# Kernel optimization log

Measured on AMD Instinct MI355X. Metric: run time of the kernel, lower is better.

The kernel has to match this reference:

```python
import jax, jax.numpy as jnp
import numpy as np

NUM_HEADS = 16
LN_EPS = 1e-5


def _layer_norm(x, w, b, eps=LN_EPS):
    m = jnp.mean(x, axis=-1, keepdims=True)
    v = jnp.var(x, axis=-1, keepdims=True)
    return (x - m) / jnp.sqrt(v + eps) * w + b


def setup_inputs() -> dict:
    key = jax.random.key(0)
    L, D, DFF, B, S = 16, 1024, 4096, 4, 1024
    ks = jax.random.split(key, 6)
    w_scale = 0.02
    return {
        "x": jax.random.normal(ks[0], (B, S, D), jnp.float32),
        "qkv_w": jax.random.normal(ks[1], (L, 3 * D, D), jnp.float32) * w_scale,
        "qkv_b": jnp.zeros((L, 3 * D), jnp.float32),
        "out_w": jax.random.normal(ks[2], (L, D, D), jnp.float32) * w_scale,
        "out_b": jnp.zeros((L, D), jnp.float32),
        "w1": jax.random.normal(ks[3], (L, DFF, D), jnp.float32) * w_scale,
        "b1": jnp.zeros((L, DFF), jnp.float32),
        "w2": jax.random.normal(ks[4], (L, D, DFF), jnp.float32) * w_scale,
        "b2": jnp.zeros((L, D), jnp.float32),
        "ln1_w": jnp.ones((L, D), jnp.float32),
        "ln1_b": jnp.zeros((L, D), jnp.float32),
        "ln2_w": jnp.ones((L, D), jnp.float32),
        "ln2_b": jnp.zeros((L, D), jnp.float32),
    }


def reference(x, qkv_w, qkv_b, out_w, out_b, w1, b1, w2, b2, ln1_w, ln1_b, ln2_w, ln2_b):
    # T2STransformer.process_prompt: stack of T2SBlocks with causal attention.
    B, S, D = x.shape
    H = NUM_HEADS
    dh = D // H
    # causal additive bias [1,1,S,S]; True on/below diagonal -> attend
    causal = jnp.tril(jnp.ones((S, S), bool))
    bias = jnp.where(causal, 0.0, -jnp.inf).astype(x.dtype)[None, None]
    scale = 1.0 / np.sqrt(dh)

    def step(h, p):
        (qw, qb, ow, ob, mw1, mb1, mw2, mb2, l1w, l1b, l2w, l2b) = p
        qkv = h @ qw.T + qb                      # [B,S,3D]
        q, k, v = jnp.split(qkv, 3, axis=-1)
        q = q.reshape(B, S, H, dh).transpose(0, 2, 1, 3)  # [B,H,S,dh]
        k = k.reshape(B, S, H, dh).transpose(0, 2, 1, 3)
        v = v.reshape(B, S, H, dh).transpose(0, 2, 1, 3)
        scores = jnp.einsum("bhqd,bhkd->bhqk", q, k) * scale + bias
        attn = jax.nn.softmax(scores, axis=-1)
        ctx = jnp.einsum("bhqk,bhkd->bhqd", attn, v)
        ctx = ctx.transpose(0, 2, 1, 3).reshape(B, S, D)
        h = h + (ctx @ ow.T + ob)
        h = _layer_norm(h, l1w, l1b)
        mlp = jax.nn.relu(h @ mw1.T + mb1) @ mw2.T + mb2
        h = _layer_norm(h + mlp, l2w, l2b)
        return h, None

    params = (qkv_w, qkv_b, out_w, out_b, w1, b1, w2, b2, ln1_w, ln1_b, ln2_w, ln2_b)
    out, _ = jax.lax.scan(step, x, params)
    return out
```

## Files before the change

kernel.cpp:

```cpp
#include <hip/hip_runtime.h>
#include <hip/hip_bf16.h>

typedef float f32x4 __attribute__((ext_vector_type(4)));
typedef __bf16 bf16x8 __attribute__((ext_vector_type(8)));
typedef unsigned short ushort_t;

__device__ __forceinline__ unsigned short f2bf(float f) {
    unsigned int u = __builtin_bit_cast(unsigned int, f);
    u += 0x7fffu + ((u >> 16) & 1u);
    return (unsigned short)(u >> 16);
}

#define GCAST(p) ((const __attribute__((address_space(1))) void*)(p))
#define LCAST(p) ((__attribute__((address_space(3))) void*)(p))

__device__ __forceinline__ bf16x8 ldsw(const unsigned short* T, int row, int bcol) {
    return *reinterpret_cast<const bf16x8*>(
        reinterpret_cast<const char*>(T) + row * 128 + (bcol ^ ((row & 7) << 4)));
}

__device__ __forceinline__ int xcd_swizzle(int bid, int nwg) {
    int cpx = nwg >> 3;
    return (bid & 7) * cpx + (bid >> 3);
}

__global__ __launch_bounds__(256) void convert_weights_kernel(
    const float* __restrict__ qw, const float* __restrict__ ow,
    const float* __restrict__ w1, const float* __restrict__ w2,
    unsigned short* __restrict__ dst)
{
    int i = blockIdx.x * 256 + threadIdx.x;
    const float* src; int off;
    if (i < 786432)       { src = qw; off = i; }
    else if (i < 1048576) { src = ow; off = i - 786432; }
    else if (i < 2097152) { src = w1; off = i - 1048576; }
    else                  { src = w2; off = i - 2097152; }
    float4 v = ((const float4*)src)[off];
    ushort4 u;
    u.x = f2bf(v.x); u.y = f2bf(v.y); u.z = f2bf(v.z); u.w = f2bf(v.w);
    ((ushort4*)dst)[i] = u;
}

__global__ __launch_bounds__(256) void gemm_kernel(
    const unsigned short* __restrict__ A, const unsigned short* __restrict__ W,
    const float* __restrict__ bias, void* __restrict__ Cout,
    int N, int K, int relu, int out_bf16)
{
    __shared__ alignas(16) unsigned short As[128][64];
    __shared__ alignas(16) unsigned short Bs[128][64];

    const int tid  = threadIdx.x;
    const int nwg  = gridDim.x * gridDim.y;
    const int swz  = xcd_swizzle(blockIdx.y * gridDim.x + blockIdx.x, nwg);
    const int bn   = swz % gridDim.x, bm = swz / gridDim.x;
    const int wave = tid >> 6, lane = tid & 63;
    const int wm   = (wave >> 1) * 64, wn = (wave & 1) * 64;
    const int l15  = lane & 15, quad = lane >> 4;
    const int srow = lane >> 3;
    const int scol = (lane & 7) * 8;

    f32x4 acc[4][4];
#pragma unroll
    for (int i = 0; i < 4; i++)
#pragma unroll
        for (int j = 0; j < 4; j++) acc[i][j] = f32x4{0.f, 0.f, 0.f, 0.f};

    const unsigned short* Abase = A + (size_t)(bm * 128) * K;
    const unsigned short* Wbase = W + (size_t)(bn * 128) * K;

    for (int k0 = 0; k0 < K; k0 += 64) {
        __syncthreads();
#pragma unroll
        for (int i = 0; i < 4; i++) {
            int r0 = (i * 4 + wave) * 8;
            __builtin_amdgcn_global_load_lds(
                GCAST(&Abase[(size_t)(r0 + srow) * K + k0 + scol]),
                LCAST(&As[r0][0]), 16, 0, 0);
            __builtin_amdgcn_global_load_lds(
                GCAST(&Wbase[(size_t)(r0 + srow) * K + k0 + scol]),
                LCAST(&Bs[r0][0]), 16, 0, 0);
        }
        __syncthreads();

#pragma unroll
        for (int ks = 0; ks < 2; ks++) {
            bf16x8 a[4], b[4];
#pragma unroll
            for (int mt = 0; mt < 4; mt++)
                a[mt] = *reinterpret_cast<const bf16x8*>(&As[wm + mt * 16 + l15][ks * 32 + quad * 8]);
#pragma unroll
            for (int nt = 0; nt < 4; nt++)
                b[nt] = *reinterpret_cast<const bf16x8*>(&Bs[wn + nt * 16 + l15][ks * 32 + quad * 8]);
#pragma unroll
            for (int mt = 0; mt < 4; mt++)
#pragma unroll
                for (int nt = 0; nt < 4; nt++)
                    acc[mt][nt] = __builtin_amdgcn_mfma_f32_16x16x32_bf16(
                        a[mt], b[nt], acc[mt][nt], 0, 0, 0);
        }
    }

    float* Cf = (float*)Cout;
    unsigned short* Cb = (unsigned short*)Cout;
#pragma unroll
    for (int nt = 0; nt < 4; nt++) {
        int gn = bn * 128 + wn + nt * 16 + l15;
        float bv = bias[gn];
#pragma unroll
        for (int mt = 0; mt < 4; mt++) {
            int gm0 = bm * 128 + wm + mt * 16 + quad * 4;
#pragma unroll
            for (int r = 0; r < 4; r++) {
                float v = acc[mt][nt][r] + bv;
                if (relu) v = fmaxf(v, 0.f);
                if (out_bf16) Cb[(size_t)(gm0 + r) * N + gn] = f2bf(v);
                else          Cf[(size_t)(gm0 + r) * N + gn] = v;
            }
        }
    }
}

__global__ __launch_bounds__(256) void gemm_splitk_kernel(
    const unsigned short* __restrict__ A, const unsigned short* __restrict__ W,
    const float* __restrict__ bias, float* __restrict__ C0, float* __restrict__ C1,
    int N, int K)
{
    __shared__ alignas(16) unsigned short As[128][64];
    __shared__ alignas(16) unsigned short Bs[128][64];

    const int tid  = threadIdx.x;
    const int nwg  = gridDim.x * gridDim.y;
    const int swz  = xcd_swizzle(blockIdx.y * gridDim.x + blockIdx.x, nwg);
    const int bn   = swz % gridDim.x, bm = swz / gridDim.x;
    const int kz   = blockIdx.z;
    const int kbeg = kz * (K >> 1);
    const int kend = kbeg + (K >> 1);
    const int wave = tid >> 6, lane = tid & 63;
    const int wm   = (wave >> 1) * 64, wn = (wave & 1) * 64;
    const int l15  = lane & 15, quad = lane >> 4;
    const int srow = lane >> 3;
    const int scol = (lane & 7) * 8;

    f32x4 acc[4][4];
#pragma unroll
    for (int i = 0; i < 4; i++)
#pragma unroll
        for (int j = 0; j < 4; j++) acc[i][j] = f32x4{0.f, 0.f, 0.f, 0.f};

    const unsigned short* Abase = A + (size_t)(bm * 128) * K;
    const unsigned short* Wbase = W + (size_t)(bn * 128) * K;

    for (int k0 = kbeg; k0 < kend; k0 += 64) {
        __syncthreads();
#pragma unroll
        for (int i = 0; i < 4; i++) {
            int r0 = (i * 4 + wave) * 8;
            __builtin_amdgcn_global_load_lds(
                GCAST(&Abase[(size_t)(r0 + srow) * K + k0 + scol]),
                LCAST(&As[r0][0]), 16, 0, 0);
            __builtin_amdgcn_global_load_lds(
                GCAST(&Wbase[(size_t)(r0 + srow) * K + k0 + scol]),
                LCAST(&Bs[r0][0]), 16, 0, 0);
        }
        __syncthreads();

#pragma unroll
        for (int ks = 0; ks < 2; ks++) {
            bf16x8 a[4], b[4];
#pragma unroll
            for (int mt = 0; mt < 4; mt++)
                a[mt] = *reinterpret_cast<const bf16x8*>(&As[wm + mt * 16 + l15][ks * 32 + quad * 8]);
#pragma unroll
            for (int nt = 0; nt < 4; nt++)
                b[nt] = *reinterpret_cast<const bf16x8*>(&Bs[wn + nt * 16 + l15][ks * 32 + quad * 8]);
#pragma unroll
            for (int mt = 0; mt < 4; mt++)
#pragma unroll
                for (int nt = 0; nt < 4; nt++)
                    acc[mt][nt] = __builtin_amdgcn_mfma_f32_16x16x32_bf16(
                        a[mt], b[nt], acc[mt][nt], 0, 0, 0);
        }
    }

    float* Cf = kz ? C1 : C0;
#pragma unroll
    for (int nt = 0; nt < 4; nt++) {
        int gn = bn * 128 + wn + nt * 16 + l15;
        float bv = kz ? 0.f : bias[gn];
#pragma unroll
        for (int mt = 0; mt < 4; mt++) {
            int gm0 = bm * 128 + wm + mt * 16 + quad * 4;
#pragma unroll
            for (int r = 0; r < 4; r++)
                Cf[(size_t)(gm0 + r) * N + gn] = acc[mt][nt][r] + bv;
        }
    }
}

__global__ __launch_bounds__(256) void attn_kernel(
    const unsigned short* __restrict__ qkv, unsigned short* __restrict__ ctx)
{
    const int qt = blockIdx.x;
    const int bh = blockIdx.y;
    const int b  = bh >> 4, h = bh & 15;
    const int tid = threadIdx.x, wave = tid >> 6, lane = tid & 63;
    const int l15 = lane & 15, quad = lane >> 4;
    const int srow = lane >> 3;
    const int scolz = ((lane & 7) ^ srow) * 8;
    const float scale = 0.125f;

    __shared__ alignas(16) unsigned short Qs[64][64];
    __shared__ alignas(16) unsigned short Ks[64][64];
    __shared__ alignas(16) unsigned short Vt[64][64];
    __shared__ alignas(16) unsigned short Ps[64][64];

    const unsigned short* qbase = qkv + (size_t)(b * 1024 + qt * 64) * 3072 + h * 64;
#pragma unroll
    for (int i = 0; i < 2; i++) {
        int r0 = (i * 4 + wave) * 8;
        __builtin_amdgcn_global_load_lds(
            GCAST(&qbase[(size_t)(r0 + srow) * 3072 + scolz]),
            LCAST(&Qs[r0][0]), 16, 0, 0);
    }

    f32x4 O[4];
#pragma unroll
    for (int dt = 0; dt < 4; dt++) O[dt] = f32x4{0.f, 0.f, 0.f, 0.f};
    float m_run[4], l_run[4];
#pragma unroll
    for (int r = 0; r < 4; r++) { m_run[r] = -__builtin_inff(); l_run[r] = 0.f; }

    const int q_row_base = qt * 64 + wave * 16;

    for (int j = 0; j <= qt; j++) {
        __syncthreads();
        const unsigned short* kbase = qkv + (size_t)(b * 1024 + j * 64) * 3072 + 1024 + h * 64;
        const unsigned short* vbase = qkv + (size_t)(b * 1024 + j * 64) * 3072 + 2048 + h * 64;
#pragma unroll
        for (int i = 0; i < 2; i++) {
            int r0 = (i * 4 + wave) * 8;
            __builtin_amdgcn_global_load_lds(
                GCAST(&kbase[(size_t)(r0 + srow) * 3072 + scolz]),
                LCAST(&Ks[r0][0]), 16, 0, 0);
        }
#pragma unroll
        for (int i = 0; i < 4; i++) {
            int idx = tid + i * 256;
            int k = idx >> 4, c4 = (idx & 15) * 4;
            ushort4 vv = *(const ushort4*)&vbase[(size_t)k * 3072 + c4];
            char* vt = (char*)Vt;
            int klo = (k & 7) * 2;
            int kch = (k >> 3) << 4;
            const unsigned short* vp = (const unsigned short*)&vv;
#pragma unroll
            for (int j2 = 0; j2 < 4; j2++) {
                int d = c4 + j2;
                *(unsigned short*)(vt + d * 128 + ((kch ^ ((d & 7) << 4)) | klo)) = vp[j2];
            }
        }
        __syncthreads();

        f32x4 Sc[4];
#pragma unroll
        for (int nt = 0; nt < 4; nt++) Sc[nt] = f32x4{0.f, 0.f, 0.f, 0.f};
        __builtin_amdgcn_s_setprio(1);
#pragma unroll
        for (int ks = 0; ks < 2; ks++) {
            bf16x8 aq = ldsw(&Qs[0][0], wave * 16 + l15, ks * 64 + quad * 16);
#pragma unroll
            for (int nt = 0; nt < 4; nt++) {
                bf16x8 bk = ldsw(&Ks[0][0], nt * 16 + l15, ks * 64 + quad * 16);
                Sc[nt] = __builtin_amdgcn_mfma_f32_16x16x32_bf16(aq, bk, Sc[nt], 0, 0, 0);
            }
        }
        __builtin_amdgcn_s_setprio(0);

#pragma unroll
        for (int nt = 0; nt < 4; nt++)
#pragma unroll
            for (int r = 0; r < 4; r++) Sc[nt][r] *= scale;

        if (j == qt) {
#pragma unroll
            for (int r = 0; r < 4; r++) {
                int qg = q_row_base + quad * 4 + r;
#pragma unroll
                for (int nt = 0; nt < 4; nt++) {
                    int kg = j * 64 + nt * 16 + l15;
                    if (kg > qg) Sc[nt][r] = -__builtin_inff();
                }
            }
        }

        float alpha[4];
#pragma unroll
        for (int r = 0; r < 4; r++) {
            float mx = -__builtin_inff();
#pragma unroll
            for (int nt = 0; nt < 4; nt++) mx = fmaxf(mx, Sc[nt][r]);
#pragma unroll
            for (int off = 1; off < 16; off <<= 1) mx = fmaxf(mx, __shfl_xor(mx, off));
            float mnew = fmaxf(m_run[r], mx);
            alpha[r] = __expf(m_run[r] - mnew);
            m_run[r] = mnew;
        }

#pragma unroll
        for (int r = 0; r < 4; r++) {
            float sum = 0.f;
#pragma unroll
            for (int nt = 0; nt < 4; nt++) {
                float p = __expf(Sc[nt][r] - m_run[r]);
                Sc[nt][r] = p;
                sum += p;
            }
#pragma unroll
            for (int off = 1; off < 16; off <<= 1) sum += __shfl_xor(sum, off);
            l_run[r] = l_run[r] * alpha[r] + sum;
        }

#pragma unroll
        for (int dt = 0; dt < 4; dt++)
#pragma unroll
            for (int r = 0; r < 4; r++) O[dt][r] *= alpha[r];

        {
            char* ps = (char*)Ps;
#pragma unroll
            for (int nt = 0; nt < 4; nt++)
#pragma unroll
                for (int r = 0; r < 4; r++) {
                    int row = wave * 16 + quad * 4 + r;
                    int col = nt * 16 + l15;
                    *(unsigned short*)(ps + row * 128 + ((col * 2) ^ ((row & 7) << 4)))
                        = f2bf(Sc[nt][r]);
                }
        }

        __builtin_amdgcn_s_setprio(1);
#pragma unroll
        for (int ks = 0; ks < 2; ks++) {
            bf16x8 ap = ldsw(&Ps[0][0], wave * 16 + l15, ks * 64 + quad * 16);
#pragma unroll
            for (int dt = 0; dt < 4; dt++) {
                bf16x8 bv = ldsw(&Vt[0][0], dt * 16 + l15, ks * 64 + quad * 16);
                O[dt] = __builtin_amdgcn_mfma_f32_16x16x32_bf16(ap, bv, O[dt], 0, 0, 0);
            }
        }
        __builtin_amdgcn_s_setprio(0);
    }

    unsigned short* obase = ctx + (size_t)(b * 1024 + qt * 64 + wave * 16) * 1024 + h * 64;
#pragma unroll
    for (int r = 0; r < 4; r++) {
        float inv = 1.f / l_run[r];
#pragma unroll
        for (int dt = 0; dt < 4; dt++)
            obase[(size_t)(quad * 4 + r) * 1024 + dt * 16 + l15] = f2bf(O[dt][r] * inv);
    }
}

__global__ __launch_bounds__(256) void ln_residual_kernel(
    float* __restrict__ h, unsigned short* __restrict__ hb,
    const float* __restrict__ r, const float* __restrict__ r2,
    const float* __restrict__ w, const float* __restrict__ b)
{
    const int row = blockIdx.x;
    const int tid = threadIdx.x;
    const int lane = tid & 63, wave = tid >> 6;

    float4 hv = *(float4*)&h[(size_t)row * 1024 + tid * 4];
    float4 rv = *(const float4*)&r[(size_t)row * 1024 + tid * 4];
    float4 r2v = *(const float4*)&r2[(size_t)row * 1024 + tid * 4];
    float x0 = hv.x + rv.x + r2v.x, x1 = hv.y + rv.y + r2v.y;
    float x2 = hv.z + rv.z + r2v.z, x3 = hv.w + rv.w + r2v.w;

    float s  = x0 + x1 + x2 + x3;
    float s2 = x0 * x0 + x1 * x1 + x2 * x2 + x3 * x3;
#pragma unroll
    for (int off = 32; off >= 1; off >>= 1) {
        s  += __shfl_xor(s, off);
        s2 += __shfl_xor(s2, off);
    }
    __shared__ float ls[4], ls2[4];
    if (lane == 0) { ls[wave] = s; ls2[wave] = s2; }
    __syncthreads();
    s  = ls[0] + ls[1] + ls[2] + ls[3];
    s2 = ls2[0] + ls2[1] + ls2[2] + ls2[3];

    const float inv_n = 1.f / 1024.f;
    float mean = s * inv_n;
    float var  = s2 * inv_n - mean * mean;
    float rstd = rsqrtf(var + 1e-5f);

    float4 wv = *(const float4*)&w[tid * 4];
    float4 bv = *(const float4*)&b[tid * 4];
    float4 out;
    out.x = (x0 - mean) * rstd * wv.x + bv.x;
    out.y = (x1 - mean) * rstd * wv.y + bv.y;
    out.z = (x2 - mean) * rstd * wv.z + bv.z;
    out.w = (x3 - mean) * rstd * wv.w + bv.w;
    *(float4*)&h[(size_t)row * 1024 + tid * 4] = out;
    ushort4 ub;
    ub.x = f2bf(out.x); ub.y = f2bf(out.y); ub.z = f2bf(out.z); ub.w = f2bf(out.w);
    *(ushort4*)&hb[(size_t)row * 1024 + tid * 4] = ub;
}

__global__ __launch_bounds__(256) void copy_convert_kernel(
    const float* __restrict__ in, float* __restrict__ h, unsigned short* __restrict__ hb)
{
    int i = blockIdx.x * 256 + threadIdx.x;
    float4 v = ((const float4*)in)[i];
    ((float4*)h)[i] = v;
    ushort4 u;
    u.x = f2bf(v.x); u.y = f2bf(v.y); u.z = f2bf(v.z); u.w = f2bf(v.w);
    ((ushort4*)hb)[i] = u;
}

extern "C" void kernel_launch(void* const* d_in, const int* in_sizes, int n_in,
                              void* d_out, int out_size, void* d_ws, size_t ws_size,
                              hipStream_t stream)
{
    const float* x     = (const float*)d_in[0];
    const float* qkv_w = (const float*)d_in[1];
    const float* qkv_b = (const float*)d_in[2];
    const float* out_w = (const float*)d_in[3];
    const float* out_b = (const float*)d_in[4];
    const float* w1    = (const float*)d_in[5];
    const float* b1    = (const float*)d_in[6];
    const float* w2    = (const float*)d_in[7];
    const float* b2    = (const float*)d_in[8];
    const float* ln1w  = (const float*)d_in[9];
    const float* ln1b  = (const float*)d_in[10];
    const float* ln2w  = (const float*)d_in[11];
    const float* ln2b  = (const float*)d_in[12];

    float* h = (float*)d_out;
    char* ws = (char*)d_ws;
    unsigned short* qkvb = (unsigned short*)ws;
    unsigned short* tb   = (unsigned short*)ws;
    unsigned short* ctxb = (unsigned short*)(ws + 33554432);
    unsigned short* hb   = (unsigned short*)(ws + 33554432 + 8388608);
    unsigned short* wbf  = (unsigned short*)(ws + 50331648);
    float*          r    = (float*)(ws + 75497472);
    float*          r2   = (float*)(ws + 92274688);

    unsigned short* wb_qkv = wbf;
    unsigned short* wb_out = wbf + 3145728;
    unsigned short* wb_w1  = wbf + 4194304;
    unsigned short* wb_w2  = wbf + 8388608;

    copy_convert_kernel<<<4096, 256, 0, stream>>>(x, h, hb);

    for (int l = 0; l < 16; l++) {
        convert_weights_kernel<<<12288, 256, 0, stream>>>(
            qkv_w + (size_t)l * 3145728, out_w + (size_t)l * 1048576,
            w1 + (size_t)l * 4194304, w2 + (size_t)l * 4194304, wbf);

        gemm_kernel<<<dim3(24, 32), 256, 0, stream>>>(
            hb, wb_qkv, qkv_b + (size_t)l * 3072, qkvb, 3072, 1024, 0, 1);
        attn_kernel<<<dim3(16, 64), 256, 0, stream>>>(qkvb, ctxb);
        gemm_splitk_kernel<<<dim3(8, 32, 2), 256, 0, stream>>>(
            ctxb, wb_out, out_b + (size_t)l * 1024, r, r2, 1024, 1024);
        ln_residual_kernel<<<4096, 256, 0, stream>>>(
            h, hb, r, r2, ln1w + (size_t)l * 1024, ln1b + (size_t)l * 1024);
        gemm_kernel<<<dim3(32, 32), 256, 0, stream>>>(
            hb, wb_w1, b1 + (size_t)l * 4096, tb, 4096, 1024, 1, 1);
        gemm_splitk_kernel<<<dim3(8, 32, 2), 256, 0, stream>>>(
            tb, wb_w2, b2 + (size_t)l * 1024, r, r2, 1024, 4096);
        ln_residual_kernel<<<4096, 256, 0, stream>>>(
            h, hb, r, r2, ln2w + (size_t)l * 1024, ln2b + (size_t)l * 1024);
    }
}
```

Baseline: 5.460 ms.

## Replace 128x128 GEMM with double-buffered 256x256 tile GEMM for QKV and FFN1

Swaps the 128x128 single-buffered GEMM for a 256x256 tile kernel with 8 waves. It double-buffers the LDS staging through async global-to-LDS loads, uses an XOR-swizzled LDS layout, and interleaves fragment loads with MFMA groups under raised wave priority. The goal is more data reuse per tile and hiding global load latency behind compute. The trade-off is fewer workgroups (192 and 256 blocks), which can leave compute units underfilled, plus 128KB of LDS per block.

```diff
diff --git a/kernel.cpp b/kernel.cpp
--- a/kernel.cpp
+++ b/kernel.cpp
@@ -41,80 +41,152 @@
     ((ushort4*)dst)[i] = u;
 }
 
-__global__ __launch_bounds__(256) void gemm_kernel(
+__global__ __launch_bounds__(512, 2) void gemm256_kernel(
     const unsigned short* __restrict__ A, const unsigned short* __restrict__ W,
-    const float* __restrict__ bias, void* __restrict__ Cout,
-    int N, int K, int relu, int out_bf16)
-{
-    __shared__ alignas(16) unsigned short As[128][64];
-    __shared__ alignas(16) unsigned short Bs[128][64];
+    const float* __restrict__ bias, unsigned short* __restrict__ C,
+    int N, int K, int relu)
+{
+    __shared__ alignas(16) unsigned short As[2][256][64];
+    __shared__ alignas(16) unsigned short Bs[2][256][64];
 
     const int tid  = threadIdx.x;
+    const int wave = tid >> 6, lane = tid & 63;
     const int nwg  = gridDim.x * gridDim.y;
     const int swz  = xcd_swizzle(blockIdx.y * gridDim.x + blockIdx.x, nwg);
     const int bn   = swz % gridDim.x, bm = swz / gridDim.x;
-    const int wave = tid >> 6, lane = tid & 63;
-    const int wm   = (wave >> 1) * 64, wn = (wave & 1) * 64;
+    const int wr   = wave >> 2;
+    const int wc   = wave & 3;
     const int l15  = lane & 15, quad = lane >> 4;
-    const int srow = lane >> 3;
-    const int scol = (lane & 7) * 8;
-
-    f32x4 acc[4][4];
-#pragma unroll
-    for (int i = 0; i < 4; i++)
+    const int srow8  = lane >> 3;
+    const int schunk = ((lane & 7) ^ srow8) * 8;
+
+    const unsigned short* Abase = A + (size_t)(bm * 256) * K;
+    const unsigned short* Wbase = W + (size_t)(bn * 256) * K;
+
+    f32x4 acc[8][4];
+#pragma unroll
+    for (int i = 0; i < 8; i++)
 #pragma unroll
         for (int j = 0; j < 4; j++) acc[i][j] = f32x4{0.f, 0.f, 0.f, 0.f};
 
-    const unsigned short* Abase = A + (size_t)(bm * 128) * K;
-    const unsigned short* Wbase = W + (size_t)(bn * 128) * K;
-
-    for (int k0 = 0; k0 < K; k0 += 64) {
-        __syncthreads();
-#pragma unroll
-        for (int i = 0; i < 4; i++) {
-            int r0 = (i * 4 + wave) * 8;
-            __builtin_amdgcn_global_load_lds(
-                GCAST(&Abase[(size_t)(r0 + srow) * K + k0 + scol]),
-                LCAST(&As[r0][0]), 16, 0, 0);
-            __builtin_amdgcn_global_load_lds(
-                GCAST(&Wbase[(size_t)(r0 + srow) * K + k0 + scol]),
-                LCAST(&Bs[r0][0]), 16, 0, 0);
-        }
-        __syncthreads();
-
-#pragma unroll
-        for (int ks = 0; ks < 2; ks++) {
-            bf16x8 a[4], b[4];
-#pragma unroll
-            for (int mt = 0; mt < 4; mt++)
-                a[mt] = *reinterpret_cast<const bf16x8*>(&As[wm + mt * 16 + l15][ks * 32 + quad * 8]);
-#pragma unroll
-            for (int nt = 0; nt < 4; nt++)
-                b[nt] = *reinterpret_cast<const bf16x8*>(&Bs[wn + nt * 16 + l15][ks * 32 + quad * 8]);
-#pragma unroll
-            for (int mt = 0; mt < 4; mt++)
-#pragma unroll
-                for (int nt = 0; nt < 4; nt++)
+    const int NT = K >> 6;
+
+#define STAGE256(buf_, t_) do {                                               \
+    int k0_ = (t_) * 64;                                                      \
+    _Pragma("unroll")                                                         \
+    for (int s = 0; s < 4; s++) {                                             \
+        __builtin_amdgcn_global_load_lds(                                     \
+            GCAST(&Abase[(size_t)(s * 64 + wave * 8 + srow8) * K + k0_ + schunk]), \
+            LCAST(&As[buf_][s * 64 + wave * 8][0]), 16, 0, 0);                \
+        __builtin_amdgcn_global_load_lds(                                     \
+            GCAST(&Wbase[(size_t)(s * 64 + wave * 8 + srow8) * K + k0_ + schunk]), \
+            LCAST(&Bs[buf_][s * 64 + wave * 8][0]), 16, 0, 0);                \
+    }                                                                         \
+} while (0)
+
+    STAGE256(0, 0);
+    STAGE256(1, 1);
+    asm volatile("s_waitcnt vmcnt(8)" ::: "memory");
+    __builtin_amdgcn_s_barrier();
+
+    for (int t = 0; t < NT; t++) {
+        const unsigned short* Al = &As[t & 1][0][0];
+        const unsigned short* Bl = &Bs[t & 1][0][0];
+        bf16x8 aA[4][2], bB0[2][2], bB1[2][2];
+
+#pragma unroll
+        for (int mt = 0; mt < 4; mt++)
+#pragma unroll
+            for (int ks = 0; ks < 2; ks++)
+                aA[mt][ks] = ldsw(Al, wr * 128 + mt * 16 + l15, ks * 64 + quad * 16);
+#pragma unroll
+        for (int nt = 0; nt < 2; nt++)
+#pragma unroll
+            for (int ks = 0; ks < 2; ks++)
+                bB0[nt][ks] = ldsw(Bl, wc * 64 + nt * 16 + l15, ks * 64 + quad * 16);
+        asm volatile("s_waitcnt lgkmcnt(0)" ::: "memory");
+        __builtin_amdgcn_sched_barrier(0);
+        __builtin_amdgcn_s_setprio(1);
+#pragma unroll
+        for (int mt = 0; mt < 4; mt++)
+#pragma unroll
+            for (int nt = 0; nt < 2; nt++)
+#pragma unroll
+                for (int ks = 0; ks < 2; ks++)
                     acc[mt][nt] = __builtin_amdgcn_mfma_f32_16x16x32_bf16(
-                        a[mt], b[nt], acc[mt][nt], 0, 0, 0);
-        }
-    }
-
-    float* Cf = (float*)Cout;
-    unsigned short* Cb = (unsigned short*)Cout;
+                        aA[mt][ks], bB0[nt][ks], acc[mt][nt], 0, 0, 0);
+        __builtin_amdgcn_s_setprio(0);
+
+#pragma unroll
+        for (int nt = 0; nt < 2; nt++)
+#pragma unroll
+            for (int ks = 0; ks < 2; ks++)
+                bB1[nt][ks] = ldsw(Bl, wc * 64 + (nt + 2) * 16 + l15, ks * 64 + quad * 16);
+        asm volatile("s_waitcnt lgkmcnt(0)" ::: "memory");
+        __builtin_amdgcn_sched_barrier(0);
+        __builtin_amdgcn_s_setprio(1);
+#pragma unroll
+        for (int mt = 0; mt < 4; mt++)
+#pragma unroll
+            for (int nt = 0; nt < 2; nt++)
+#pragma unroll
+                for (int ks = 0; ks < 2; ks++)
+                    acc[mt][nt + 2] = __builtin_amdgcn_mfma_f32_16x16x32_bf16(
+                        aA[mt][ks], bB1[nt][ks], acc[mt][nt + 2], 0, 0, 0);
+        __builtin_amdgcn_s_setprio(0);
+
+#pragma unroll
+        for (int mt = 0; mt < 4; mt++)
+#pragma unroll
+            for (int ks = 0; ks < 2; ks++)
+                aA[mt][ks] = ldsw(Al, wr * 128 + (mt + 4) * 16 + l15, ks * 64 + quad * 16);
+        asm volatile("s_waitcnt lgkmcnt(0)" ::: "memory");
+        __builtin_amdgcn_sched_barrier(0);
+        __builtin_amdgcn_s_setprio(1);
+#pragma unroll
+        for (int mt = 0; mt < 4; mt++)
+#pragma unroll
+            for (int nt = 0; nt < 2; nt++)
+#pragma unroll
+                for (int ks = 0; ks < 2; ks++)
+                    acc[mt + 4][nt + 2] = __builtin_amdgcn_mfma_f32_16x16x32_bf16(
+                        aA[mt][ks], bB1[nt][ks], acc[mt + 4][nt + 2], 0, 0, 0);
+        __builtin_amdgcn_s_setprio(0);
+
+        __builtin_amdgcn_s_setprio(1);
+#pragma unroll
+        for (int mt = 0; mt < 4; mt++)
+#pragma unroll
+            for (int nt = 0; nt < 2; nt++)
+#pragma unroll
+                for (int ks = 0; ks < 2; ks++)
+                    acc[mt + 4][nt] = __builtin_amdgcn_mfma_f32_16x16x32_bf16(
+                        aA[mt][ks], bB0[nt][ks], acc[mt + 4][nt], 0, 0, 0);
+        __builtin_amdgcn_s_setprio(0);
+
+        __builtin_amdgcn_s_barrier();
+        if (t + 2 < NT) {
+            STAGE256(t & 1, t + 2);
+            asm volatile("s_waitcnt vmcnt(8)" ::: "memory");
+        } else {
+            asm volatile("s_waitcnt vmcnt(0)" ::: "memory");
+        }
+        __builtin_amdgcn_s_barrier();
+    }
+#undef STAGE256
+
 #pragma unroll
     for (int nt = 0; nt < 4; nt++) {
-        int gn = bn * 128 + wn + nt * 16 + l15;
+        int gn = bn * 256 + wc * 64 + nt * 16 + l15;
         float bv = bias[gn];
 #pragma unroll
-        for (int mt = 0; mt < 4; mt++) {
-            int gm0 = bm * 128 + wm + mt * 16 + quad * 4;
+        for (int mt = 0; mt < 8; mt++) {
+            int gm0 = bm * 256 + wr * 128 + mt * 16 + quad * 4;
 #pragma unroll
             for (int r = 0; r < 4; r++) {
                 float v = acc[mt][nt][r] + bv;
                 if (relu) v = fmaxf(v, 0.f);
-                if (out_bf16) Cb[(size_t)(gm0 + r) * N + gn] = f2bf(v);
-                else          Cf[(size_t)(gm0 + r) * N + gn] = v;
+                C[(size_t)(gm0 + r) * N + gn] = f2bf(v);
             }
         }
     }
@@ -457,15 +529,15 @@
             qkv_w + (size_t)l * 3145728, out_w + (size_t)l * 1048576,
             w1 + (size_t)l * 4194304, w2 + (size_t)l * 4194304, wbf);
 
-        gemm_kernel<<<dim3(24, 32), 256, 0, stream>>>(
-            hb, wb_qkv, qkv_b + (size_t)l * 3072, qkvb, 3072, 1024, 0, 1);
+        gemm256_kernel<<<dim3(12, 16), 512, 0, stream>>>(
+            hb, wb_qkv, qkv_b + (size_t)l * 3072, qkvb, 3072, 1024, 0);
         attn_kernel<<<dim3(16, 64), 256, 0, stream>>>(qkvb, ctxb);
         gemm_splitk_kernel<<<dim3(8, 32, 2), 256, 0, stream>>>(
             ctxb, wb_out, out_b + (size_t)l * 1024, r, r2, 1024, 1024);
         ln_residual_kernel<<<4096, 256, 0, stream>>>(
             h, hb, r, r2, ln1w + (size_t)l * 1024, ln1b + (size_t)l * 1024);
-        gemm_kernel<<<dim3(32, 32), 256, 0, stream>>>(
-            hb, wb_w1, b1 + (size_t)l * 4096, tb, 4096, 1024, 1, 1);
+        gemm256_kernel<<<dim3(16, 16), 512, 0, stream>>>(
+            hb, wb_w1, b1 + (size_t)l * 4096, tb, 4096, 1024, 1);
         gemm_splitk_kernel<<<dim3(8, 32, 2), 256, 0, stream>>>(
             tb, wb_w2, b2 + (size_t)l * 1024, r, r2, 1024, 4096);
         ln_residual_kernel<<<4096, 256, 0, stream>>>(
```

New measurement: 4.981 ms. 8.8% less time.
